# Optimization experiments

Hardware: AMD Instinct MI355X
Metric: run time of the kernel (lower is better)

## Reference

```python
import jax, jax.numpy as jnp
import numpy as np
from jax import lax

B_SZ, D_SPEC, P, NC, MLP_D = 4096, 30, 9, 64, 64
L = P * P + 1  # 82 tokens (81 spiral + cls)


def _spiral_idx(patch=P):
    # Replicates Scan.forward's hardcoded assignments_map: center pixel, then
    # concentric rings (top row, right col, bottom row, left col), each of length 2r.
    cen = patch // 2
    rows, cols = [cen], [cen]
    for r in range(1, cen + 1):
        rows += [cen - r] * (2 * r); cols += list(range(cen - r + 1, cen + r + 1))
        rows += list(range(cen - r + 1, cen + r + 1)); cols += [cen + r] * (2 * r)
        rows += [cen + r] * (2 * r); cols += list(range(cen - r, cen + r))
        rows += list(range(cen - r, cen + r)); cols += [cen - r] * (2 * r)
    return np.asarray(rows), np.asarray(cols)

_ROWS, _COLS = _spiral_idx()


def _ln(x, g, b, eps=1e-5):
    m = x.mean(-1, keepdims=True)
    v = ((x - m) ** 2).mean(-1, keepdims=True)
    return (x - m) * lax.rsqrt(v + eps) * g + b


def _bn(x, g, b, m, v, nspatial, eps=1e-5):
    sh = (1, -1) + (1,) * nspatial
    return (x - m.reshape(sh)) * lax.rsqrt(v.reshape(sh) + eps) * g.reshape(sh) + b.reshape(sh)


def setup_inputs():
    key = jax.random.key(0)
    ks = iter(jax.random.split(key, 40))
    def rn(shape, s=0.1):
        return s * jax.random.normal(next(ks), shape, jnp.float32)
    return {
        "input_data": jax.random.normal(next(ks), (B_SZ, 1, D_SPEC, P, P), jnp.float32),
        "w3": rn((8, 1, 3, 3, 3)), "b3": rn((8,)),
        "g3": 1.0 + rn((8,)), "be3": rn((8,)), "m3": jnp.zeros((8,)), "v3": jnp.ones((8,)),
        "w2c": rn((NC, 8 * D_SPEC, 3, 3)), "b2c": rn((NC,)),
        "g2": 1.0 + rn((NC,)), "be2": rn((NC,)), "m2": jnp.zeros((NC,)), "v2": jnp.ones((NC,)),
        "pos_emb": rn((1, L, NC)), "cls_tok": rn((1, 1, NC)),
        "ln1_g": jnp.ones((NC,)), "ln1_b": jnp.zeros((NC,)),
        "Wb": rn((NC, NC)), "bb": rn((NC,)),
        "Wc": rn((NC, NC)), "bc": rn((NC,)),
        "Wd": rn((NC, NC)), "bd": rn((NC,)),
        "delta_p": rn((1, L, NC)), "A_p": rn((L, NC)),
        "Wst": rn((NC, NC)), "bst": rn((NC,)), "bias_st": rn((1, 1, NC)),
        "ln2_g": jnp.ones((NC,)), "ln2_b": jnp.zeros((NC,)),
        "Wm1": rn((NC, MLP_D)), "bm1": rn((MLP_D,)),
        "Wm2": rn((MLP_D, NC)), "bm2": rn((NC,)),
    }


def _forward(input_data, w3, b3, g3, be3, m3, v3, w2c, b2c, g2, be2, m2, v2,
             pos_emb, cls_tok, ln1_g, ln1_b, Wb, bb, Wc, bc, Wd, bd,
             delta_p, A_p, Wst, bst, bias_st, ln2_g, ln2_b, Wm1, bm1, Wm2, bm2):
    b = input_data.shape[0]
    # conv3d (SAME, k=3) + BN(eval) + ReLU
    h = lax.conv_general_dilated(input_data, w3, (1, 1, 1), [(1, 1)] * 3,
                                 dimension_numbers=("NCDHW", "OIDHW", "NCDHW"))
    h = jax.nn.relu(_bn(h + b3[None, :, None, None, None], g3, be3, m3, v3, 3))
    h = h.reshape(b, 8 * D_SPEC, P, P)  # 'b c h w y -> b (c h) w y'
    # conv2d (SAME, k=3) + BN(eval) + ReLU
    h = lax.conv_general_dilated(h, w2c, (1, 1), [(1, 1)] * 2,
                                 dimension_numbers=("NCHW", "OIHW", "NCHW"))
    h = jax.nn.relu(_bn(h + b2c[None, :, None, None], g2, be2, m2, v2, 2))
    # spiral scan gather: [B,C,H,W] -> [B,81,C]
    seq = jnp.transpose(h, (0, 2, 3, 1))[:, _ROWS, _COLS, :]
    tok = jnp.concatenate([jnp.broadcast_to(cls_tok, (b, 1, NC)), seq], axis=1) + pos_emb
    # (emb dropout = identity in eval)
    # --- Residual(LayerNormalize(S6_noC)) ---
    xn = _ln(tok, ln1_g, ln1_b)
    z = jax.nn.sigmoid(xn)
    B0 = xn @ Wb + bb
    C_ = xn @ Wc + bc
    sq = jnp.mean(xn, axis=1, keepdims=True)              # SToken squeeze [B,1,D]
    sq = jax.nn.sigmoid(jax.nn.relu(sq @ Wst + bst))
    T_ = (sq + bias_st) * xn                              # [B,L,D]
    delta = jax.nn.sigmoid(xn @ Wd + bd + delta_p)
    A_ = delta * A_p[None]                                # [B,L,D]
    Bx = delta * B0 * xn                                  # B_ * x fused
    def step(s, inp):
        a, bx, c, t = inp
        s = a * s + bx
        return s, c * s + t
    ins = (jnp.moveaxis(A_, 1, 0), jnp.moveaxis(Bx, 1, 0),
           jnp.moveaxis(C_, 1, 0), jnp.moveaxis(T_, 1, 0))  # [L,B,D]
    _, out = lax.scan(step, jnp.zeros((b, NC), xn.dtype), ins)
    tok = tok + jnp.moveaxis(out, 0, 1) * z               # residual
    # AdaptiveAvgPool1d(1) over seq + squeeze -> [B, D]
    pooled = tok.mean(axis=1)
    # --- Residual(LayerNormalize(MLP_Block)) (dropout = identity) ---
    yn = _ln(pooled, ln2_g, ln2_b)
    mlp = jax.nn.gelu(yn @ Wm1 + bm1, approximate=False) @ Wm2 + bm2
    return pooled + mlp


def reference(input_data, w3, b3, g3, be3, m3, v3, w2c, b2c, g2, be2, m2, v2,
              pos_emb, cls_tok, ln1_g, ln1_b, Wb, bb, Wc, bc, Wd, bd,
              delta_p, A_p, Wst, bst, bias_st, ln2_g, ln2_b, Wm1, bm1, Wm2, bm2):
    return _forward(input_data, w3, b3, g3, be3, m3, v3, w2c, b2c, g2, be2, m2, v2,
                    pos_emb, cls_tok, ln1_g, ln1_b, Wb, bb, Wc, bc, Wd, bd,
                    delta_p, A_p, Wst, bst, bias_st, ln2_g, ln2_b, Wm1, bm1, Wm2, bm2)
```

## Files before the change

kernel.cpp:

```cpp
#include <hip/hip_runtime.h>

typedef unsigned short u16;
typedef unsigned int u32;
typedef __attribute__((ext_vector_type(8))) short bf16x8;
typedef __attribute__((ext_vector_type(4))) float f32x4;
typedef __attribute__((ext_vector_type(4))) int i32x4;

#define DEV __device__ __forceinline__

DEV u16 f2bf(float f){
  unsigned u = __float_as_uint(f);
  u += 0x7fffu + ((u >> 16) & 1u);
  return (u16)(u >> 16);
}
DEV float bf2f(u16 h){ return __uint_as_float(((unsigned)h) << 16); }

DEV int spiral_t(int pix){
  int px = pix / 9, py = pix % 9;
  int dr = px - 4, dc = py - 4;
  int ar = dr < 0 ? -dr : dr, ac = dc < 0 ? -dc : dc;
  int r = ar > ac ? ar : ac;
  if (r == 0) return 0;
  int start = 1 + 4*r*(r-1);
  if (dr == -r && dc >= -r+1) return start + dc + r - 1;
  if (dc == r)  return start + 2*r + dr + r - 1;
  if (dr == r)  return start + 4*r + dc + r;
  return start + 6*r + dr + r;
}

__global__ __launch_bounds__(256) void k_conv3d(const float* __restrict__ x,
    const float* __restrict__ w3, const float* __restrict__ b3,
    const float* __restrict__ g3, const float* __restrict__ be3,
    const float* __restrict__ m3, const float* __restrict__ v3,
    const float* __restrict__ w2c, const float* __restrict__ g2,
    const float* __restrict__ v2,
    u16* __restrict__ h1, u16* __restrict__ Wt2){
  __shared__ float tile[3993];
  __shared__ float wle[216];
  __shared__ float sc[8], sh[8];
  int b = blockIdx.x, tid = threadIdx.x;

  if (b >= 4096){
    int idx = (b - 4096)*256 + tid;
    int kk = idx & 31;
    int o  = (idx >> 5) & 63;
    int tile2 = idx >> 11;
    int dxy = tile2 >> 3;
    int chunk = tile2 & 7;
    int ch = chunk*32 + kk;
    float v = 0.f;
    if (ch < 240){
      float s2 = g2[o] * rsqrtf(v2[o] + 1e-5f);
      v = w2c[(o*240 + ch)*9 + dxy] * s2;
    }
    Wt2[idx] = f2bf(v);
    return;
  }

  for (int i = tid; i < 3993; i += 256) tile[i] = 0.f;
  if (tid < 216) wle[tid] = w3[tid];
  if (tid < 8){
    float s = g3[tid]*rsqrtf(v3[tid]+1e-5f);
    sc[tid] = s;
    sh[tid] = (b3[tid]-m3[tid])*s + be3[tid];
  }
  __syncthreads();
  const float* xin = x + b*2430;
  for (int i = tid; i < 2430; i += 256){
    int dd = i / 81, rem = i % 81;
    int px = rem / 9, py = rem % 9;
    tile[(dd+1)*121 + (px+1)*11 + (py+1)] = xin[i];
  }
  __syncthreads();
  u16* hb = h1 + (size_t)b*19440;

  for (int col = tid; col < 648; col += 256){
    int pix = col >> 3, co = col & 7;
    int px = pix / 9, py = pix % 9;
    const float* base = tile + px*11 + py;
    float wp[27];
    #pragma unroll
    for (int q=0;q<27;q++) wp[q] = wle[co*27+q];
    float scv = sc[co], shv = sh[co];

    float s0[9], s1[9], s2[9];
#define LSL(S, SL)                                                            \
    { const float* tp2 = base + (SL)*121;                                     \
      _Pragma("unroll")                                                       \
      for (int kx=0;kx<3;kx++)                                                \
        _Pragma("unroll")                                                     \
        for (int ky=0;ky<3;ky++) S[kx*3+ky] = tp2[kx*11+ky]; }
#define DOT3(A, SA, SB, SC)                                                   \
    { A = 0.f;                                                                \
      _Pragma("unroll")                                                       \
      for (int q=0;q<9;q++) A = fmaf(SA[q], wp[q], A);                        \
      _Pragma("unroll")                                                       \
      for (int q=0;q<9;q++) A = fmaf(SB[q], wp[9+q], A);                      \
      _Pragma("unroll")                                                       \
      for (int q=0;q<9;q++) A = fmaf(SC[q], wp[18+q], A); }

    LSL(s0, 0); LSL(s1, 1); LSL(s2, 2);
    u16 outv[30];
    #pragma unroll
    for (int d3 = 0; d3 < 30; d3 += 3){
      float a;
      DOT3(a, s0, s1, s2);
      outv[d3] = f2bf(fmaxf(fmaf(a, scv, shv), 0.f));
      LSL(s0, d3+3);
      DOT3(a, s1, s2, s0);
      outv[d3+1] = f2bf(fmaxf(fmaf(a, scv, shv), 0.f));
      LSL(s1, d3+4);
      DOT3(a, s2, s0, s1);
      outv[d3+2] = f2bf(fmaxf(fmaf(a, scv, shv), 0.f));
      LSL(s2, d3+5);
    }
#undef LSL
#undef DOT3
    u32* dst = (u32*)(hb + pix*240 + co*30);
    #pragma unroll
    for (int q=0;q<15;q++) dst[q] = ((u32)outv[2*q+1] << 16) | (u32)outv[2*q];
  }
}

__global__ __launch_bounds__(256, 2) void k_conv2d(const u16* __restrict__ h1,
    const u16* __restrict__ Wt2,
    const float* __restrict__ b2c, const float* __restrict__ g2,
    const float* __restrict__ be2, const float* __restrict__ m2,
    const float* __restrict__ v2,
    const float* __restrict__ pos_emb, const float* __restrict__ cls_tok,
    const float* __restrict__ ln1_g, const float* __restrict__ ln1_b,
    const float* __restrict__ Wst, const float* __restrict__ bst,
    const float* __restrict__ bias_st,
    const float* __restrict__ Wb, const float* __restrict__ Wc,
    const float* __restrict__ Wd,
    const float* __restrict__ bbv, const float* __restrict__ bcv,
    const float* __restrict__ bdv,
    const float* __restrict__ delta_p, const float* __restrict__ A_p,
    const float* __restrict__ ln2_g, const float* __restrict__ ln2_b,
    const float* __restrict__ Wm1, const float* __restrict__ bm1,
    const float* __restrict__ Wm2, const float* __restrict__ bm2,
    float* __restrict__ out){
  __shared__ __align__(16) char smem[80848];
  const int ZROW = 80352;
  const int TSUML = 24576, SQSL = 25088, AXo = 25600, BXo = 38272, CXo = 50944;
  const int PTo = 63616, PXo = 65664, XSo = 67712;
  int tid = threadIdx.x;
  int wv = tid >> 6, ln = tid & 63;
  int lq = ln >> 4, lr = ln & 15;
  int img0 = blockIdx.x*2;
  size_t grow0 = (size_t)img0*81;

  int bln = lr*32 + lq*8;

#define LOADB(TAP, C, B)                                                        \
    { const u16* Bt_ = Wt2 + (TAP)*16384 + bln;                                 \
      _Pragma("unroll")                                                         \
      for (int kk=0;kk<2;kk++)                                                  \
        _Pragma("unroll")                                                       \
        for (int j=0;j<4;j++)                                                   \
          B[kk][j] = *(const bf16x8*)(Bt_ + ((C)*2+kk)*2048 + j*512); }

  bf16x8 bB0[2][4], bB1[2][4], bB2[2][4];
  LOADB(0, 0, bB0);
  LOADB(0, 1, bB1);
  LOADB(0, 2, bB2);

  for (int r = tid; r < 162; r += 256)
    *(i32x4*)(smem + r*496 + 480) = (i32x4){0,0,0,0};
  if (tid < 31) *(i32x4*)(smem + ZROW + tid*16) = (i32x4){0,0,0,0};
  {
    const u16* src = h1 + grow0*240;
    for (int idx = tid; idx < 162*30; idx += 256){
      int r = idx / 30, c = idx % 30;
      *(i32x4*)(smem + r*496 + c*16) = *(const i32x4*)(src + idx*8);
    }
  }
  __syncthreads();

  f32x4 acc[3][4];
  #pragma unroll
  for (int i=0;i<3;i++)
    #pragma unroll
    for (int j=0;j<4;j++) acc[i][j] = (f32x4){0.f,0.f,0.f,0.f};

#define CALCADDR(TAP, A0, A1, A13)                                              \
  { int dx = (TAP)/3 - 1, dy = (TAP)%3 - 1;                                     \
    _Pragma("unroll")                                                           \
    for (int rt=0;rt<3;rt++){                                                   \
      int row = (wv*3+rt)*16 + lr;                                              \
      int pix = row % 81;                                                       \
      int px = pix/9, py = pix%9;                                               \
      int px2 = px + dx, py2 = py + dy;                                         \
      bool valid = (row < 162) && ((unsigned)px2 < 9u) && ((unsigned)py2 < 9u); \
      int nrow = (row - pix) + px2*9 + py2;                                     \
      int base = valid ? nrow*496 : ZROW;                                       \
      A0[rt]  = base + lq*16;                                                   \
      A1[rt]  = base + 64 + lq*16;                                              \
      A13[rt] = (lq == 3) ? ZROW : (A1[rt] + 384);                              \
    } }

#define LOADA(C, SA0, SA1, SA13, A0, A1)                                        \
    { _Pragma("unroll")                                                         \
      for (int rt=0;rt<3;rt++){                                                 \
        A0[rt] = *(const bf16x8*)(smem + SA0[rt] + (C)*128);                    \
        A1[rt] = *(const bf16x8*)(smem + ((C)==3 ? SA13[rt]                     \
                                                 : SA1[rt] + (C)*128)); } }

#define DOMFMA(B, A0, A1)                                                       \
    { __builtin_amdgcn_s_setprio(1);                                            \
      _Pragma("unroll")                                                         \
      for (int rt=0;rt<3;rt++)                                                  \
        _Pragma("unroll")                                                       \
        for (int j=0;j<4;j++)                                                   \
          acc[rt][j] = __builtin_amdgcn_mfma_f32_16x16x32_bf16(A0[rt], B[0][j], acc[rt][j], 0, 0, 0); \
      _Pragma("unroll")                                                         \
      for (int rt=0;rt<3;rt++)                                                  \
        _Pragma("unroll")                                                       \
        for (int j=0;j<4;j++)                                                   \
          acc[rt][j] = __builtin_amdgcn_mfma_f32_16x16x32_bf16(A1[rt], B[1][j], acc[rt][j], 0, 0, 0); \
      __builtin_amdgcn_s_setprio(0); }

#define TAPBODY(TAPV, BA, BB, BC)                                               \
  { int ntap_ = (TAPV) < 8 ? (TAPV)+1 : 8;                                      \
    DOMFMA(BA, aAX0, aAX1);                                                     \
    LOADB((TAPV), 3, BA); LOADA(2, aC0, aC1, aC13, aAX0, aAX1);                 \
    DOMFMA(BB, aAY0, aAY1);                                                     \
    LOADB(ntap_, 0, BB); CALCADDR(ntap_, aN0, aN1, aN13);                       \
    LOADA(3, aC0, aC1, aC13, aAY0, aAY1);                                       \
    DOMFMA(BC, aAX0, aAX1);                                                     \
    LOADB(ntap_, 1, BC); LOADA(0, aN0, aN1, aN13, aAX0, aAX1);                  \
    DOMFMA(BA, aAY0, aAY1);                                                     \
    LOADB(ntap_, 2, BA); LOADA(1, aN0, aN1, aN13, aAY0, aAY1);                  \
    _Pragma("unroll")                                                           \
    for (int rt=0;rt<3;rt++){ aC0[rt]=aN0[rt]; aC1[rt]=aN1[rt]; aC13[rt]=aN13[rt]; } }

  int aC0[3], aC1[3], aC13[3];
  int aN0[3], aN1[3], aN13[3];
  bf16x8 aAX0[3], aAX1[3], aAY0[3], aAY1[3];

  CALCADDR(0, aC0, aC1, aC13);
  LOADA(0, aC0, aC1, aC13, aAX0, aAX1);
  LOADA(1, aC0, aC1, aC13, aAY0, aAY1);

  for (int t3 = 0; t3 < 9; t3 += 3){
    TAPBODY(t3+0, bB0, bB1, bB2);
    TAPBODY(t3+1, bB1, bB2, bB0);
    TAPBODY(t3+2, bB2, bB0, bB1);
  }
#undef CALCADDR
#undef LOADB
#undef LOADA
#undef DOMFMA
#undef TAPBODY

  __syncthreads();

  if (tid < 224){
    int im = tid / 112, r2 = tid % 112;
    int rr = 82 + (r2 >> 3), c = r2 & 7;
    *(i32x4*)(smem + im*12288 + rr*128 + ((c*16) ^ ((rr&7)<<4))) = (i32x4){0,0,0,0};
  }

  float t2c[4], lg[4], lb[4];
  #pragma unroll
  for (int j=0;j<4;j++){
    int col = j*16 + lr;
    float s2 = g2[col]*rsqrtf(v2[col]+1e-5f);
    t2c[j] = (b2c[col]-m2[col])*s2 + be2[col];
    lg[j] = ln1_g[col]; lb[j] = ln1_b[col];
  }

  float st0[4]={0,0,0,0}, st1[4]={0,0,0,0};
  float sx0[4]={0,0,0,0}, sx1[4]={0,0,0,0};

  #pragma unroll
  for (int rt=0;rt<3;rt++){
    #pragma unroll
    for (int e=0;e<4;e++){
      int row = (wv*3+rt)*16 + lq*4 + e;
      if (row < 162){
        int im = (row >= 81);
        int pix = row - im*81;
        int tsp = spiral_t(pix);
        const float* pe = pos_emb + (1+tsp)*64;
        float y[4], m1 = 0.f, m2v = 0.f;
        #pragma unroll
        for (int j=0;j<4;j++){
          y[j] = fmaxf(acc[rt][j][e] + t2c[j], 0.f) + pe[j*16+lr];
          m1 += y[j]; m2v = fmaf(y[j], y[j], m2v);
        }
        #pragma unroll
        for (int off=1; off<16; off<<=1){
          m1  += __shfl_xor(m1,  off, 64);
          m2v += __shfl_xor(m2v, off, 64);
        }
        float mean = m1*(1.f/64.f);
        float var  = m2v*(1.f/64.f) - mean*mean;
        float rs = rsqrtf(var + 1e-5f);
        int trow = 1 + tsp;
        char* dl = smem + im*12288 + trow*128;
        int sz = (trow & 7) << 4;
        #pragma unroll
        for (int j=0;j<4;j++){
          float xnv = (y[j]-mean)*rs*lg[j] + lb[j];
          *(u16*)(dl + (((j*16+lr)*2) ^ sz)) = f2bf(xnv);
          if (im == 0){ st0[j] += y[j]; sx0[j] += xnv; }
          else        { st1[j] += y[j]; sx1[j] += xnv; }
        }
      }
    }
  }

  #pragma unroll
  for (int j=0;j<4;j++){
    st0[j] += __shfl_xor(st0[j],16,64); st0[j] += __shfl_xor(st0[j],32,64);
    st1[j] += __shfl_xor(st1[j],16,64); st1[j] += __shfl_xor(st1[j],32,64);
    sx0[j] += __shfl_xor(sx0[j],16,64); sx0[j] += __shfl_xor(sx0[j],32,64);
    sx1[j] += __shfl_xor(sx1[j],16,64); sx1[j] += __shfl_xor(sx1[j],32,64);
  }
  float* partT = (float*)(smem + PTo);
  float* partX = (float*)(smem + PXo);
  float* xsumL = (float*)(smem + XSo);
  float* tsumL = (float*)(smem + TSUML);
  float* sqsL  = (float*)(smem + SQSL);
  if (lq == 0){
    #pragma unroll
    for (int j=0;j<4;j++){
      partT[wv*128 +       j*16+lr] = st0[j];
      partT[wv*128 + 64  + j*16+lr] = st1[j];
      partX[wv*128 +       j*16+lr] = sx0[j];
      partX[wv*128 + 64  + j*16+lr] = sx1[j];
    }
  }
  __syncthreads();
  if (tid < 128){
    int im = tid >> 6, d = tid & 63;
    float tt = partT[im*64+d] + partT[128+im*64+d] + partT[256+im*64+d] + partT[384+im*64+d];
    float xx = partX[im*64+d] + partX[128+im*64+d] + partX[256+im*64+d] + partX[384+im*64+d];
    float clsv = cls_tok[d] + pos_emb[d];
    float c1v = clsv, c2v = clsv*clsv;
    #pragma unroll
    for (int off=1; off<64; off<<=1){ c1v += __shfl_xor(c1v, off, 64); c2v += __shfl_xor(c2v, off, 64); }
    float cm = c1v*(1.f/64.f), cv = c2v*(1.f/64.f) - cm*cm;
    float cxn = (clsv - cm)*rsqrtf(cv + 1e-5f)*ln1_g[d] + ln1_b[d];
    *(u16*)(smem + im*12288 + d*2) = f2bf(cxn);
    tsumL[im*64 + d] = tt + clsv;
    xsumL[im*64 + d] = (xx + cxn) * (1.f/82.f);
  }
  __syncthreads();
  {
    int im = tid >> 7, d2 = tid & 127;
    int d = d2 >> 1, half = d2 & 1;
    float a = 0.f;
    int k0 = half*32;
    #pragma unroll
    for (int k=0;k<32;k++) a = fmaf(xsumL[im*64 + k0+k], Wst[(k0+k)*64+d], a);
    a += __shfl_xor(a, 1, 64);
    if (half == 0){
      a += bst[d];
      a = fmaxf(a, 0.f);
      a = 1.f/(1.f + __expf(-a));
      sqsL[im*64 + d] = a + bias_st[d];
    }
  }
  __syncthreads();

  bf16x8 bfr[3][2];
  {
    int cc = wv*16 + lr;
    const float* Ws[3] = {Wb, Wc, Wd};
    #pragma unroll
    for (int w=0;w<3;w++)
      #pragma unroll
      for (int kk=0;kk<2;kk++){
        int k0 = kk*32 + lq*8;
        bf16x8 f;
        #pragma unroll
        for (int e=0;e<8;e++) f[e] = (short)f2bf(Ws[w][(k0+e)*64 + cc]);
        bfr[w][kk] = f;
      }
  }
  u16* AxL = (u16*)(smem + AXo);
  u16* BxL = (u16*)(smem + BXo);
  u16* CxL = (u16*)(smem + CXo);

  for (int im = 0; im < 2; im++){
    const char* xb = smem + im*12288;
    f32x4 facc[6][3];
    #pragma unroll
    for (int i=0;i<6;i++)
      #pragma unroll
      for (int w=0;w<3;w++) facc[i][w] = (f32x4){0.f,0.f,0.f,0.f};

    #pragma unroll
    for (int rt=0;rt<6;rt++){
      int row = rt*16 + lr;
      bf16x8 afr[2];
      #pragma unroll
      for (int kk=0;kk<2;kk++)
        afr[kk] = *(const bf16x8*)(xb + row*128 + ((kk*64 + lq*16) ^ ((row&7)<<4)));
      #pragma unroll
      for (int kk=0;kk<2;kk++)
        #pragma unroll
        for (int w=0;w<3;w++)
          facc[rt][w] = __builtin_amdgcn_mfma_f32_16x16x32_bf16(afr[kk], bfr[w][kk], facc[rt][w], 0, 0, 0);
    }

    {
      int d = wv*16 + lr;
      float bB = bbv[d], bC = bcv[d], bD = bdv[d];
      #pragma unroll
      for (int rt=0;rt<6;rt++){
        #pragma unroll
        for (int e=0;e<4;e++){
          int t = rt*16 + lq*4 + e;
          if (t < 82){
            float B0 = facc[rt][0][e] + bB;
            float Cv = facc[rt][1][e] + bC;
            float Dr = facc[rt][2][e] + bD + delta_p[t*64+d];
            float D  = 1.f/(1.f + __expf(-Dr));
            float xv = bf2f(*(const u16*)(xb + t*128 + ((d*2) ^ ((t&7)<<4))));
            AxL[t*66+d] = f2bf(D * A_p[t*64+d]);
            BxL[t*66+d] = f2bf(D * B0 * xv);
            CxL[t*66+d] = f2bf(Cv);
          }
        }
      }
    }
    __syncthreads();

    if (wv == 0){
      int d = ln;
      float sq = sqsL[im*64 + d];
      float s = 0.f, racc = 0.f;
      for (int t = 0; t < 82; t++){
        float a  = bf2f(AxL[t*66+d]);
        float bx = bf2f(BxL[t*66+d]);
        float c  = bf2f(CxL[t*66+d]);
        float xv = bf2f(*(const u16*)(xb + t*128 + ((d*2) ^ ((t&7)<<4))));
        s = fmaf(a, s, bx);
        float o = fmaf(c, s, sq*xv);
        float z = 1.f/(1.f + __expf(-xv));
        racc = fmaf(o, z, racc);
      }
      float pooled = (tsumL[im*64 + d] + racc) * (1.f/82.f);
      float s1 = pooled, s2v = pooled*pooled;
      #pragma unroll
      for (int off=32; off>0; off>>=1){ s1 += __shfl_xor(s1, off, 64); s2v += __shfl_xor(s2v, off, 64); }
      float mean = s1*(1.f/64.f), var = s2v*(1.f/64.f) - mean*mean;
      float yn = (pooled - mean)*rsqrtf(var + 1e-5f)*ln2_g[d] + ln2_b[d];
      float a1 = bm1[d];
      for (int k=0;k<64;k++) a1 = fmaf(__shfl(yn, k, 64), Wm1[k*64+d], a1);
      float hg = 0.5f*a1*(1.f + erff(a1*0.70710678118654752f));
      float a2 = bm2[d];
      for (int k=0;k<64;k++) a2 = fmaf(__shfl(hg, k, 64), Wm2[k*64+d], a2);
      out[(size_t)(img0+im)*64 + d] = pooled + a2;
    }
    __syncthreads();
  }
}

extern "C" void kernel_launch(void* const* d_in, const int* in_sizes, int n_in,
                              void* d_out, int out_size, void* d_ws, size_t ws_size,
                              hipStream_t stream){
  const float* x       = (const float*)d_in[0];
  const float* w3      = (const float*)d_in[1];
  const float* b3      = (const float*)d_in[2];
  const float* g3      = (const float*)d_in[3];
  const float* be3     = (const float*)d_in[4];
  const float* m3      = (const float*)d_in[5];
  const float* v3      = (const float*)d_in[6];
  const float* w2c     = (const float*)d_in[7];
  const float* b2c     = (const float*)d_in[8];
  const float* g2      = (const float*)d_in[9];
  const float* be2     = (const float*)d_in[10];
  const float* m2      = (const float*)d_in[11];
  const float* v2      = (const float*)d_in[12];
  const float* pos_emb = (const float*)d_in[13];
  const float* cls_tok = (const float*)d_in[14];
  const float* ln1_g   = (const float*)d_in[15];
  const float* ln1_b   = (const float*)d_in[16];
  const float* Wb      = (const float*)d_in[17];
  const float* bbv     = (const float*)d_in[18];
  const float* Wc      = (const float*)d_in[19];
  const float* bc      = (const float*)d_in[20];
  const float* Wd      = (const float*)d_in[21];
  const float* bd      = (const float*)d_in[22];
  const float* delta_p = (const float*)d_in[23];
  const float* A_p     = (const float*)d_in[24];
  const float* Wst     = (const float*)d_in[25];
  const float* bst     = (const float*)d_in[26];
  const float* bias_st = (const float*)d_in[27];
  const float* ln2_g   = (const float*)d_in[28];
  const float* ln2_b   = (const float*)d_in[29];
  const float* Wm1     = (const float*)d_in[30];
  const float* bm1     = (const float*)d_in[31];
  const float* Wm2     = (const float*)d_in[32];
  const float* bm2     = (const float*)d_in[33];

  char* ws = (char*)d_ws;
  u16*   h1   = (u16*)ws;
  u16*   Wt2  = (u16*)(ws + 159252480);

  k_conv3d<<<4672, 256, 0, stream>>>(x, w3, b3, g3, be3, m3, v3,
                                     w2c, g2, v2, h1, Wt2);
  k_conv2d<<<2048, 256, 0, stream>>>(h1, Wt2, b2c, g2, be2, m2, v2,
                                     pos_emb, cls_tok, ln1_g, ln1_b,
                                     Wst, bst, bias_st,
                                     Wb, Wc, Wd, bbv, bc, bd, delta_p, A_p,
                                     ln2_g, ln2_b, Wm1, bm1, Wm2, bm2,
                                     (float*)d_out);
}
```

Before: 361.7 us.

## Parallelize selective scan across four waves with chunked prefix combine

The 82-step sequential scan previously ran on a single wave while the other three idled. It now splits the sequence into four chunks, one per wave. Each wave first computes its chunk's product and affine offset, then rebuilds its starting state from the earlier chunks' summaries and runs its own chunk. Partial residual sums are reduced through shared memory, and the LayerNorm plus MLP tail is deferred so two waves handle both images at the end. This adds an extra pass over A/Bx, an extra barrier, and reuses existing shared-memory regions (PTo/PXo) as scratch, which risks aliasing.

```diff
diff --git a/kernel.cpp b/kernel.cpp
--- a/kernel.cpp
+++ b/kernel.cpp
@@ -383,6 +383,8 @@
   u16* AxL = (u16*)(smem + AXo);
   u16* BxL = (u16*)(smem + BXo);
   u16* CxL = (u16*)(smem + CXo);
+  float* RCl = (float*)(smem + PTo);
+  float* PQl = (float*)(smem + PXo);
 
   for (int im = 0; im < 2; im++){
     const char* xb = smem + im*12288;
@@ -429,11 +431,31 @@
     }
     __syncthreads();
 
-    if (wv == 0){
+    {
       int d = ln;
+      int S = wv*21, E = (wv==3) ? 82 : S+21;
+      float P = 1.f, Q = 0.f;
+      for (int t = S; t < E; t++){
+        float a  = bf2f(AxL[t*66+d]);
+        float bx = bf2f(BxL[t*66+d]);
+        Q = fmaf(a, Q, bx);
+        P *= a;
+      }
+      PQl[(wv*2+0)*64 + d] = P;
+      PQl[(wv*2+1)*64 + d] = Q;
+    }
+    __syncthreads();
+    {
+      int d = ln;
+      int S = wv*21, E = (wv==3) ? 82 : S+21;
+      float s = 0.f;
+      #pragma unroll
+      for (int w2 = 0; w2 < 3; w2++)
+        if (w2 < wv)
+          s = fmaf(PQl[(w2*2+0)*64 + d], s, PQl[(w2*2+1)*64 + d]);
       float sq = sqsL[im*64 + d];
-      float s = 0.f, racc = 0.f;
-      for (int t = 0; t < 82; t++){
+      float racc = 0.f;
+      for (int t = S; t < E; t++){
         float a  = bf2f(AxL[t*66+d]);
         float bx = bf2f(BxL[t*66+d]);
         float c  = bf2f(CxL[t*66+d]);
@@ -443,20 +465,27 @@
         float z = 1.f/(1.f + __expf(-xv));
         racc = fmaf(o, z, racc);
       }
-      float pooled = (tsumL[im*64 + d] + racc) * (1.f/82.f);
-      float s1 = pooled, s2v = pooled*pooled;
-      #pragma unroll
-      for (int off=32; off>0; off>>=1){ s1 += __shfl_xor(s1, off, 64); s2v += __shfl_xor(s2v, off, 64); }
-      float mean = s1*(1.f/64.f), var = s2v*(1.f/64.f) - mean*mean;
-      float yn = (pooled - mean)*rsqrtf(var + 1e-5f)*ln2_g[d] + ln2_b[d];
-      float a1 = bm1[d];
-      for (int k=0;k<64;k++) a1 = fmaf(__shfl(yn, k, 64), Wm1[k*64+d], a1);
-      float hg = 0.5f*a1*(1.f + erff(a1*0.70710678118654752f));
-      float a2 = bm2[d];
-      for (int k=0;k<64;k++) a2 = fmaf(__shfl(hg, k, 64), Wm2[k*64+d], a2);
-      out[(size_t)(img0+im)*64 + d] = pooled + a2;
+      RCl[im*256 + wv*64 + d] = racc;
     }
     __syncthreads();
+  }
+
+  if (tid < 128){
+    int im = wv, d = ln;
+    float racc = RCl[im*256 + d] + RCl[im*256 + 64 + d]
+               + RCl[im*256 + 128 + d] + RCl[im*256 + 192 + d];
+    float pooled = (tsumL[im*64 + d] + racc) * (1.f/82.f);
+    float s1 = pooled, s2v = pooled*pooled;
+    #pragma unroll
+    for (int off=32; off>0; off>>=1){ s1 += __shfl_xor(s1, off, 64); s2v += __shfl_xor(s2v, off, 64); }
+    float mean = s1*(1.f/64.f), var = s2v*(1.f/64.f) - mean*mean;
+    float yn = (pooled - mean)*rsqrtf(var + 1e-5f)*ln2_g[d] + ln2_b[d];
+    float a1 = bm1[d];
+    for (int k=0;k<64;k++) a1 = fmaf(__shfl(yn, k, 64), Wm1[k*64+d], a1);
+    float hg = 0.5f*a1*(1.f + erff(a1*0.70710678118654752f));
+    float a2 = bm2[d];
+    for (int k=0;k<64;k++) a2 = fmaf(__shfl(hg, k, 64), Wm2[k*64+d], a2);
+    out[(size_t)(img0+im)*64 + d] = pooled + a2;
   }
 }
 
```

Result: faster. 333.0 us (-7.9%).
